# Performance work log

Measured on AMD Instinct MI355X. Metric: run time of the kernel, lower is better.

Reference implementation:

```python
import jax, jax.numpy as jnp
import numpy as np

INPUT_DIM = 3
NUM_LEVELS = 8
LEVEL_DIM = 2
SCALE = 2
BASE_RES = 16
MAX_PARAMS = 2 ** 19
INDEX_PARAMS = 2 ** 14
PROBE = 2 ** 4
BATCH = 524288


def _level_offsets():
    offsets, off = [], 0
    for i in range(NUM_LEVELS):
        res = int(np.ceil(BASE_RES * SCALE ** i))
        p = min(MAX_PARAMS, res ** INPUT_DIM)
        p = int(np.ceil(p / 32) * 32)
        off += p
        offsets.append(off)
    return offsets

OFFSETS = _level_offsets()           # cumulative embedding offsets per level
TOTAL_EMB = OFFSETS[-1]              # 2920448
TOTAL_CB = NUM_LEVELS * INDEX_PARAMS # 131072

PRIMES1 = np.array([1, 2654435761, 805459861], dtype=np.uint32)
PRIMES2 = np.array([1, 2654435767, 805459871], dtype=np.uint32)
_neig = np.arange(1 << INPUT_DIM, dtype=np.int64)[:, None]
_dims = np.arange(INPUT_DIM, dtype=np.int64)[None, :]
BIN_MASK = (_neig & (1 << _dims)) == 0  # [8, 3]


def _fast_hash(ind_u32, primes, size):
    # uint32 multiply wraps mod 2^32, matching `* primes & 0xFFFFFFFF` in torch
    h = ind_u32 * jnp.asarray(primes)
    acc = h[..., 0]
    for d in range(1, INPUT_DIM):
        acc = acc ^ h[..., d]
    return (acc % jnp.uint32(size)).astype(jnp.int32)


def setup_inputs() -> dict:
    key = jax.random.key(0)
    k1, k2, k3 = jax.random.split(key, 3)
    inputs = jax.random.uniform(k1, (BATCH, INPUT_DIM), dtype=jnp.float32)
    # xavier_uniform bounds
    b_e = float(np.sqrt(6.0 / (TOTAL_EMB + LEVEL_DIM)))
    b_c = float(np.sqrt(6.0 / (TOTAL_CB + PROBE)))
    embeddings = jax.random.uniform(k2, (TOTAL_EMB, LEVEL_DIM), jnp.float32, -b_e, b_e)
    code_book = jax.random.uniform(k3, (TOTAL_CB, PROBE), jnp.float32, -b_c, b_c)
    return {"inputs": inputs, "embeddings": embeddings, "code_book": code_book}


def reference(inputs, embeddings, code_book):
    bin_mask = jnp.asarray(BIN_MASK)                    # [8, 3]
    probe_idx = jnp.arange(PROBE, dtype=jnp.int32)      # [PROBE]
    outs = []
    for i in range(NUM_LEVELS):
        res = int(np.ceil(BASE_RES * SCALE ** i))
        offset = 0 if i == 0 else OFFSETS[i - 1]
        params = OFFSETS[i] - offset
        index_offset = i * INDEX_PARAMS
        x = inputs * res
        xi = jnp.floor(x).astype(jnp.int32)             # inputs >= 0, trunc == floor
        xf = x - xi.astype(x.dtype)
        xi = xi[:, None, :]                             # [B, 1, 3]
        xf = xf[:, None, :]
        neigs = jnp.where(bin_mask, xi, xi + 1).astype(jnp.uint32)  # [B, 8, 3]
        # soft index probing (training path)
        h2 = _fast_hash(neigs, PRIMES2, INDEX_PARAMS) + index_offset  # [B, 8]
        index_feat = code_book[h2]                                    # [B, 8, PROBE]
        index_w = jax.nn.softmax(index_feat, axis=-1)
        h1 = _fast_hash(neigs, PRIMES1, params) * PROBE               # [B, 8]
        h1 = (h1[..., None] + probe_idx) % params + offset            # [B, 8, PROBE]
        nf = embeddings[h1]                                           # [B, 8, PROBE, 2]
        feat = jnp.sum(nf * index_w[..., None], axis=-2)              # [B, 8, 2]
        # trilinear interpolation weights
        w = jnp.prod(jnp.where(bin_mask, 1.0 - xf, xf), axis=-1, keepdims=True)  # [B, 8, 1]
        outs.append(jnp.sum(feat * w, axis=-2))                       # [B, 2]
    return jnp.concatenate(outs, axis=-1)                             # [B, 16]
```

## Files before the change

### kernel.cpp

```cpp
#include <hip/hip_runtime.h>
#include <hip/hip_fp16.h>

#define PRIME1Y 2654435761u
#define PRIME1Z 805459861u
#define PRIME2Y 2654435767u
#define PRIME2Z 805459871u

template<int CTRL>
__device__ __forceinline__ float dpp_add(float x) {
    int xi = __float_as_int(x);
    int yi = __builtin_amdgcn_update_dpp(0, xi, CTRL, 0xf, 0xf, true);
    return x + __int_as_float(yi);
}
#define DPP_QUAD_XOR1 0xB1
#define DPP_QUAD_XOR2 0x4E
#define DPP_HALF_MIR  0x141
#define DPP_ROW_MIR   0x140

__device__ __forceinline__ __half2 hc(unsigned u) {
    return __builtin_bit_cast(__half2, u);
}
__device__ __forceinline__ float texp(float x) {
    return fmaf(x, fmaf(x, 0.5f, 1.f), 1.f);
}

__global__ __launch_bounds__(256) void cvt_kernel(
    const float* __restrict__ emb, const float* __restrict__ cb,
    __half* __restrict__ embh, __half* __restrict__ wcb,
    int n4e, int nrows)
{
    int i = blockIdx.x * 256 + threadIdx.x;
    if (i < n4e) {
        float4 v = *reinterpret_cast<const float4*>(emb + (size_t)i * 4);
        __half2 a = __floats2half2_rn(v.x, v.y);
        __half2 b = __floats2half2_rn(v.z, v.w);
        uint2 pk;
        pk.x = __builtin_bit_cast(unsigned, a);
        pk.y = __builtin_bit_cast(unsigned, b);
        *reinterpret_cast<uint2*>(embh + (size_t)i * 4) = pk;
        return;
    }
    i -= n4e;
    if (i >= nrows) return;
    const float* rp = cb + (size_t)i * 16;
    float e[16];
    float S = 0.f;
    #pragma unroll
    for (int k = 0; k < 16; ++k) { e[k] = texp(rp[k]); S += e[k]; }
    const float r = 1.0f / S;
    uint4 lo, hi;
    unsigned w[8];
    #pragma unroll
    for (int k = 0; k < 8; ++k) {
        __half2 h = __floats2half2_rn(e[2*k] * r, e[2*k+1] * r);
        w[k] = __builtin_bit_cast(unsigned, h);
    }
    lo.x = w[0]; lo.y = w[1]; lo.z = w[2]; lo.w = w[3];
    hi.x = w[4]; hi.y = w[5]; hi.z = w[6]; hi.w = w[7];
    char* dst = reinterpret_cast<char*>(wcb) + (size_t)i * 32;
    *reinterpret_cast<uint4*>(dst) = lo;
    *reinterpret_cast<uint4*>(dst + 16) = hi;
}

__global__ __launch_bounds__(256) void compact_hash_f16(
    const float* __restrict__ in,
    const __half* __restrict__ embh,
    const __half* __restrict__ wcb,
    float* __restrict__ out)
{
    const unsigned lane = threadIdx.x & 63u;
    const unsigned wave = threadIdx.x >> 6;
    const unsigned L    = blockIdx.x & 7u;
    const unsigned t = lane & 1u;
    const unsigned c = (lane >> 1) & 7u;
    const unsigned p = lane >> 4;

    const float res = (float)(16u << L);
    const unsigned kb_raw = 12u + 3u * L;
    const unsigned kb = kb_raw < 19u ? kb_raw : 19u;
    const unsigned pmask = (1u << kb) - 1u;
    const unsigned offset = (L == 0u) ? 0u :
                            (L == 1u) ? 4096u :
                            (L == 2u) ? 36864u :
                            299008u + (L - 3u) * 524288u;

    unsigned pb = (blockIdx.x >> 3) * 16u + wave * 4u;
    pb = (unsigned)__builtin_amdgcn_readfirstlane((int)pb);
    const float* ip = in + (size_t)pb * 3u;
    const float ax = ip[0], ay = ip[1],  az = ip[2];
    const float bx = ip[3], by = ip[4],  bz = ip[5];
    const float ex = ip[6], ey = ip[7],  ez = ip[8];
    const float dx = ip[9], dy = ip[10], dz = ip[11];
    const bool hi0 = (lane & 16u) != 0u;
    const bool hi1 = (lane & 32u) != 0u;
    const float xin = hi1 ? (hi0 ? dx : ex) : (hi0 ? bx : ax);
    const float yin = hi1 ? (hi0 ? dy : ey) : (hi0 ? by : ay);
    const float zin = hi1 ? (hi0 ? dz : ez) : (hi0 ? bz : az);

    const float sx = xin * res, sy = yin * res, sz = zin * res;
    const float fx0 = floorf(sx), fy0 = floorf(sy), fz0 = floorf(sz);
    const float fx = sx - fx0, fy = sy - fy0, fz = sz - fz0;
    const unsigned ux = (unsigned)(int)fx0;
    const unsigned uy = (unsigned)(int)fy0;
    const unsigned uz = (unsigned)(int)fz0;

    const unsigned cx = ux + (c & 1u);
    const unsigned hy = uy * PRIME1Y + ((c & 2u) ? PRIME1Y : 0u);
    const unsigned hz = uz * PRIME1Z + ((c & 4u) ? PRIME1Z : 0u);
    const unsigned gy = uy * PRIME2Y + ((c & 2u) ? PRIME2Y : 0u);
    const unsigned gz = uz * PRIME2Z + ((c & 4u) ? PRIME2Z : 0u);

    const unsigned h1 = (cx ^ hy ^ hz) & pmask;
    const unsigned h2 = ((cx ^ gy ^ gz) & 16383u) + (L << 14);

    const uint4 craw = *reinterpret_cast<const uint4*>(
        reinterpret_cast<const char*>(wcb) + h2 * 32u + t * 16u);
    const unsigned erow = offset + ((h1 << 4) & pmask);
    const char* ep = reinterpret_cast<const char*>(embh) + erow * 4u + t * 32u;
    const uint4 eraw0 = *reinterpret_cast<const uint4*>(ep);
    const uint4 eraw1 = *reinterpret_cast<const uint4*>(ep + 16);

    const __half2 w01 = hc(craw.x), w23 = hc(craw.y);
    const __half2 w45 = hc(craw.z), w67 = hc(craw.w);

    __half2 f01 =        __hmul2(__half2half2(__low2half (w01)), hc(eraw0.x));
    f01 = __hfma2(__half2half2(__high2half(w01)), hc(eraw0.y), f01);
    f01 = __hfma2(__half2half2(__low2half (w23)), hc(eraw0.z), f01);
    f01 = __hfma2(__half2half2(__high2half(w23)), hc(eraw0.w), f01);
    f01 = __hfma2(__half2half2(__low2half (w45)), hc(eraw1.x), f01);
    f01 = __hfma2(__half2half2(__high2half(w45)), hc(eraw1.y), f01);
    f01 = __hfma2(__half2half2(__low2half (w67)), hc(eraw1.z), f01);
    f01 = __hfma2(__half2half2(__high2half(w67)), hc(eraw1.w), f01);

    const float wt = ((c & 1u) ? fx : 1.f - fx)
                   * ((c & 2u) ? fy : 1.f - fy)
                   * ((c & 4u) ? fz : 1.f - fz);

    float g0 = __half2float(__low2half(f01))  * wt;
    float g1 = __half2float(__high2half(f01)) * wt;
    g0 = dpp_add<DPP_QUAD_XOR1>(g0);
    g0 = dpp_add<DPP_QUAD_XOR2>(g0);
    g0 = dpp_add<DPP_HALF_MIR>(g0);
    g0 = dpp_add<DPP_ROW_MIR>(g0);
    g1 = dpp_add<DPP_QUAD_XOR1>(g1);
    g1 = dpp_add<DPP_QUAD_XOR2>(g1);
    g1 = dpp_add<DPP_HALF_MIR>(g1);
    g1 = dpp_add<DPP_ROW_MIR>(g1);

    if ((lane & 15u) == 0u) {
        *reinterpret_cast<float2*>(
            reinterpret_cast<char*>(out) + (pb + p) * 64u + L * 8u) =
            make_float2(g0, g1);
    }
}

__device__ __forceinline__ float4 ld4(const float* p) {
    return *reinterpret_cast<const float4*>(p);
}
#define DPP_BCAST15   0x142
__global__ __launch_bounds__(256) void compact_hash_f32(
    const float* __restrict__ in,
    const float* __restrict__ emb,
    const float* __restrict__ cb,
    float* __restrict__ out)
{
    const unsigned lane = threadIdx.x & 63u;
    const unsigned wave = threadIdx.x >> 6;
    const unsigned L    = blockIdx.x & 7u;
    const unsigned point = (blockIdx.x >> 3) * 8u + wave * 2u + (lane >> 5);
    const unsigned s = lane & 3u;
    const unsigned c = (lane >> 2) & 7u;
    const float res = (float)(16u << L);
    const unsigned kb_raw = 12u + 3u * L;
    const unsigned kb = kb_raw < 19u ? kb_raw : 19u;
    const unsigned pmask = (1u << kb) - 1u;
    const unsigned offset = (L == 0u) ? 0u : (L == 1u) ? 4096u :
                            (L == 2u) ? 36864u : 299008u + (L - 3u) * 524288u;
    const float xin = in[point * 3u + 0u];
    const float yin = in[point * 3u + 1u];
    const float zin = in[point * 3u + 2u];
    const float sx = xin * res, sy = yin * res, sz = zin * res;
    const float fx0 = floorf(sx), fy0 = floorf(sy), fz0 = floorf(sz);
    const float fx = sx - fx0, fy = sy - fy0, fz = sz - fz0;
    const unsigned ux = (unsigned)(int)fx0;
    const unsigned uy = (unsigned)(int)fy0;
    const unsigned uz = (unsigned)(int)fz0;
    const unsigned cx = ux + (c & 1u);
    const unsigned hy = uy * PRIME1Y + ((c & 2u) ? PRIME1Y : 0u);
    const unsigned hz = uz * PRIME1Z + ((c & 4u) ? PRIME1Z : 0u);
    const unsigned gy = uy * PRIME2Y + ((c & 2u) ? PRIME2Y : 0u);
    const unsigned gz = uz * PRIME2Z + ((c & 4u) ? PRIME2Z : 0u);
    const unsigned h1 = (cx ^ hy ^ hz) & pmask;
    const unsigned h2 = ((cx ^ gy ^ gz) & 16383u) + (L << 14);
    const float4 cw = ld4(cb + (size_t)h2 * 16u + s * 4u);
    const unsigned ebase = (offset + ((h1 << 4) & pmask)) * 2u;
    const float* ep = emb + (size_t)ebase + s * 8u;
    const float4 e01 = ld4(ep);
    const float4 e23 = ld4(ep + 4);
    const float w0 = texp(cw.x), w1 = texp(cw.y);
    const float w2 = texp(cw.z), w3 = texp(cw.w);
    float S = (w0 + w1) + (w2 + w3);
    S = dpp_add<DPP_QUAD_XOR1>(S);
    S = dpp_add<DPP_QUAD_XOR2>(S);
    float f0 = w0 * e01.x,    f1 = w0 * e01.y;
    f0 = fmaf(w1, e01.z, f0); f1 = fmaf(w1, e01.w, f1);
    f0 = fmaf(w2, e23.x, f0); f1 = fmaf(w2, e23.y, f1);
    f0 = fmaf(w3, e23.z, f0); f1 = fmaf(w3, e23.w, f1);
    const float wt = ((c & 1u) ? fx : 1.f - fx)
                   * ((c & 2u) ? fy : 1.f - fy)
                   * ((c & 4u) ? fz : 1.f - fz);
    const float r = wt * __builtin_amdgcn_rcpf(S);
    float g0 = f0 * r, g1 = f1 * r;
    g0 = dpp_add<DPP_QUAD_XOR1>(g0); g0 = dpp_add<DPP_QUAD_XOR2>(g0);
    g0 = dpp_add<DPP_HALF_MIR>(g0);  g0 = dpp_add<DPP_ROW_MIR>(g0);
    g0 = dpp_add<DPP_BCAST15>(g0);
    g1 = dpp_add<DPP_QUAD_XOR1>(g1); g1 = dpp_add<DPP_QUAD_XOR2>(g1);
    g1 = dpp_add<DPP_HALF_MIR>(g1);  g1 = dpp_add<DPP_ROW_MIR>(g1);
    g1 = dpp_add<DPP_BCAST15>(g1);
    if ((lane & 31u) == 16u) {
        *reinterpret_cast<float2*>(
            reinterpret_cast<char*>(out) + point * 64u + L * 8u) =
            make_float2(g0, g1);
    }
}

extern "C" void kernel_launch(void* const* d_in, const int* in_sizes, int n_in,
                              void* d_out, int out_size, void* d_ws, size_t ws_size,
                              hipStream_t stream) {
    const float* in  = (const float*)d_in[0];
    const float* emb = (const float*)d_in[1];
    const float* cb  = (const float*)d_in[2];
    float* out = (float*)d_out;

    const int batch = in_sizes[0] / 3;
    const size_t embh_bytes = (size_t)in_sizes[1] * 2;
    const size_t cbh_bytes  = (size_t)in_sizes[2] * 2;

    if (ws_size >= embh_bytes + cbh_bytes) {
        __half* embh = (__half*)d_ws;
        __half* wcb  = (__half*)((char*)d_ws + embh_bytes);
        const int n4e   = in_sizes[1] / 4;
        const int nrows = in_sizes[2] / 16;
        const int ncvt = n4e + nrows;
        hipLaunchKernelGGL(cvt_kernel, dim3((ncvt + 255) / 256), dim3(256),
                           0, stream, emb, cb, embh, wcb, n4e, nrows);
        const int nblocks = (batch / 16) * 8;
        hipLaunchKernelGGL(compact_hash_f16, dim3(nblocks), dim3(256),
                           0, stream, in, embh, wcb, out);
    } else {
        const int nblocks = (batch / 8) * 8;
        hipLaunchKernelGGL(compact_hash_f32, dim3(nblocks), dim3(256),
                           0, stream, in, emb, cb, out);
    }
}
```

Baseline: 221.8 us.

## Remap lanes to z-pair corners and store duplicated half2 softmax weights

Each lane now handles two corners that differ only in z, covering a quarter of the 16 probes instead of half of one corner's probes. Softmax weights are stored pre-duplicated as half2 pairs in a 64-byte-per-row workspace layout, so the FMA chain reads packed weights directly with no broadcast shuffles. Per-lane loads become two 16-byte embedding loads plus two codebook loads, and the x/y hash terms are shared between the two corners. The change doubles codebook workspace size and traffic, and falls back to the 32-byte layout when the workspace is too small.

```diff
diff --git a/kernel.cpp b/kernel.cpp
--- a/kernel.cpp
+++ b/kernel.cpp
@@ -20,6 +20,9 @@
 __device__ __forceinline__ __half2 hc(unsigned u) {
     return __builtin_bit_cast(__half2, u);
 }
+__device__ __forceinline__ unsigned hb(__half2 h) {
+    return __builtin_bit_cast(unsigned, h);
+}
 __device__ __forceinline__ float texp(float x) {
     return fmaf(x, fmaf(x, 0.5f, 1.f), 1.f);
 }
@@ -27,16 +30,14 @@
 __global__ __launch_bounds__(256) void cvt_kernel(
     const float* __restrict__ emb, const float* __restrict__ cb,
     __half* __restrict__ embh, __half* __restrict__ wcb,
-    int n4e, int nrows)
+    int n4e, int nrows, int dup)
 {
     int i = blockIdx.x * 256 + threadIdx.x;
     if (i < n4e) {
         float4 v = *reinterpret_cast<const float4*>(emb + (size_t)i * 4);
-        __half2 a = __floats2half2_rn(v.x, v.y);
-        __half2 b = __floats2half2_rn(v.z, v.w);
         uint2 pk;
-        pk.x = __builtin_bit_cast(unsigned, a);
-        pk.y = __builtin_bit_cast(unsigned, b);
+        pk.x = hb(__floats2half2_rn(v.x, v.y));
+        pk.y = hb(__floats2half2_rn(v.z, v.w));
         *reinterpret_cast<uint2*>(embh + (size_t)i * 4) = pk;
         return;
     }
@@ -48,20 +49,32 @@
     #pragma unroll
     for (int k = 0; k < 16; ++k) { e[k] = texp(rp[k]); S += e[k]; }
     const float r = 1.0f / S;
-    uint4 lo, hi;
-    unsigned w[8];
-    #pragma unroll
-    for (int k = 0; k < 8; ++k) {
-        __half2 h = __floats2half2_rn(e[2*k] * r, e[2*k+1] * r);
-        w[k] = __builtin_bit_cast(unsigned, h);
-    }
-    lo.x = w[0]; lo.y = w[1]; lo.z = w[2]; lo.w = w[3];
-    hi.x = w[4]; hi.y = w[5]; hi.z = w[6]; hi.w = w[7];
-    char* dst = reinterpret_cast<char*>(wcb) + (size_t)i * 32;
-    *reinterpret_cast<uint4*>(dst) = lo;
-    *reinterpret_cast<uint4*>(dst + 16) = hi;
-}
-
+    if (dup) {
+        char* dst = reinterpret_cast<char*>(wcb) + (size_t)i * 64;
+        #pragma unroll
+        for (int k = 0; k < 4; ++k) {
+            uint4 v;
+            v.x = hb(__floats2half2_rn(e[4*k+0]*r, e[4*k+0]*r));
+            v.y = hb(__floats2half2_rn(e[4*k+1]*r, e[4*k+1]*r));
+            v.z = hb(__floats2half2_rn(e[4*k+2]*r, e[4*k+2]*r));
+            v.w = hb(__floats2half2_rn(e[4*k+3]*r, e[4*k+3]*r));
+            *reinterpret_cast<uint4*>(dst + k * 16) = v;
+        }
+    } else {
+        char* dst = reinterpret_cast<char*>(wcb) + (size_t)i * 32;
+        #pragma unroll
+        for (int k = 0; k < 2; ++k) {
+            uint4 v;
+            v.x = hb(__floats2half2_rn(e[8*k+0]*r, e[8*k+1]*r));
+            v.y = hb(__floats2half2_rn(e[8*k+2]*r, e[8*k+3]*r));
+            v.z = hb(__floats2half2_rn(e[8*k+4]*r, e[8*k+5]*r));
+            v.w = hb(__floats2half2_rn(e[8*k+6]*r, e[8*k+7]*r));
+            *reinterpret_cast<uint4*>(dst + k * 16) = v;
+        }
+    }
+}
+
+template<bool DUP>
 __global__ __launch_bounds__(256) void compact_hash_f16(
     const float* __restrict__ in,
     const __half* __restrict__ embh,
@@ -71,14 +84,15 @@
     const unsigned lane = threadIdx.x & 63u;
     const unsigned wave = threadIdx.x >> 6;
     const unsigned L    = blockIdx.x & 7u;
-    const unsigned t = lane & 1u;
-    const unsigned c = (lane >> 1) & 7u;
+    const unsigned s = lane & 3u;
+    const unsigned q = (lane >> 2) & 3u;
     const unsigned p = lane >> 4;
 
     const float res = (float)(16u << L);
     const unsigned kb_raw = 12u + 3u * L;
     const unsigned kb = kb_raw < 19u ? kb_raw : 19u;
     const unsigned pmask = (1u << kb) - 1u;
+    const unsigned pm4 = pmask >> 4;
     const unsigned offset = (L == 0u) ? 0u :
                             (L == 1u) ? 4096u :
                             (L == 2u) ? 36864u :
@@ -104,40 +118,65 @@
     const unsigned uy = (unsigned)(int)fy0;
     const unsigned uz = (unsigned)(int)fz0;
 
-    const unsigned cx = ux + (c & 1u);
-    const unsigned hy = uy * PRIME1Y + ((c & 2u) ? PRIME1Y : 0u);
-    const unsigned hz = uz * PRIME1Z + ((c & 4u) ? PRIME1Z : 0u);
-    const unsigned gy = uy * PRIME2Y + ((c & 2u) ? PRIME2Y : 0u);
-    const unsigned gz = uz * PRIME2Z + ((c & 4u) ? PRIME2Z : 0u);
-
-    const unsigned h1 = (cx ^ hy ^ hz) & pmask;
-    const unsigned h2 = ((cx ^ gy ^ gz) & 16383u) + (L << 14);
-
-    const uint4 craw = *reinterpret_cast<const uint4*>(
-        reinterpret_cast<const char*>(wcb) + h2 * 32u + t * 16u);
-    const unsigned erow = offset + ((h1 << 4) & pmask);
-    const char* ep = reinterpret_cast<const char*>(embh) + erow * 4u + t * 32u;
-    const uint4 eraw0 = *reinterpret_cast<const uint4*>(ep);
-    const uint4 eraw1 = *reinterpret_cast<const uint4*>(ep + 16);
-
-    const __half2 w01 = hc(craw.x), w23 = hc(craw.y);
-    const __half2 w45 = hc(craw.z), w67 = hc(craw.w);
-
-    __half2 f01 =        __hmul2(__half2half2(__low2half (w01)), hc(eraw0.x));
-    f01 = __hfma2(__half2half2(__high2half(w01)), hc(eraw0.y), f01);
-    f01 = __hfma2(__half2half2(__low2half (w23)), hc(eraw0.z), f01);
-    f01 = __hfma2(__half2half2(__high2half(w23)), hc(eraw0.w), f01);
-    f01 = __hfma2(__half2half2(__low2half (w45)), hc(eraw1.x), f01);
-    f01 = __hfma2(__half2half2(__high2half(w45)), hc(eraw1.y), f01);
-    f01 = __hfma2(__half2half2(__low2half (w67)), hc(eraw1.z), f01);
-    f01 = __hfma2(__half2half2(__high2half(w67)), hc(eraw1.w), f01);
-
-    const float wt = ((c & 1u) ? fx : 1.f - fx)
-                   * ((c & 2u) ? fy : 1.f - fy)
-                   * ((c & 4u) ? fz : 1.f - fz);
-
-    float g0 = __half2float(__low2half(f01))  * wt;
-    float g1 = __half2float(__high2half(f01)) * wt;
+    const unsigned cx  = ux + (q & 1u);
+    const unsigned hxy = cx ^ (uy * PRIME1Y + ((q & 2u) ? PRIME1Y : 0u));
+    const unsigned gxy = cx ^ (uy * PRIME2Y + ((q & 2u) ? PRIME2Y : 0u));
+    const unsigned hz0 = uz * PRIME1Z, hz1 = hz0 + PRIME1Z;
+    const unsigned gz0 = uz * PRIME2Z, gz1 = gz0 + PRIME2Z;
+
+    const unsigned cbase = DUP ? ((L << 20) + s * 16u) : ((L << 19) + s * 8u);
+    const unsigned ebase = offset * 4u + s * 16u;
+
+    const unsigned h2a = (gxy ^ gz0) & 16383u;
+    const unsigned h2b = (gxy ^ gz1) & 16383u;
+    const unsigned ca = cbase + (DUP ? (h2a << 6) : (h2a << 5));
+    const unsigned cbo = cbase + (DUP ? (h2b << 6) : (h2b << 5));
+    const unsigned ea = ebase + (((hxy ^ hz0) & pm4) << 6);
+    const unsigned eb = ebase + (((hxy ^ hz1) & pm4) << 6);
+
+    const char* cbp = reinterpret_cast<const char*>(wcb);
+    const char* ebp = reinterpret_cast<const char*>(embh);
+    const uint4 eA = *reinterpret_cast<const uint4*>(ebp + ea);
+    const uint4 eB = *reinterpret_cast<const uint4*>(ebp + eb);
+
+    __half2 f01A, f01B;
+    if (DUP) {
+        const uint4 cA = *reinterpret_cast<const uint4*>(cbp + ca);
+        const uint4 cB = *reinterpret_cast<const uint4*>(cbp + cbo);
+        f01A =        __hmul2(hc(cA.x), hc(eA.x));
+        f01A = __hfma2(hc(cA.y), hc(eA.y), f01A);
+        f01A = __hfma2(hc(cA.z), hc(eA.z), f01A);
+        f01A = __hfma2(hc(cA.w), hc(eA.w), f01A);
+        f01B =        __hmul2(hc(cB.x), hc(eB.x));
+        f01B = __hfma2(hc(cB.y), hc(eB.y), f01B);
+        f01B = __hfma2(hc(cB.z), hc(eB.z), f01B);
+        f01B = __hfma2(hc(cB.w), hc(eB.w), f01B);
+    } else {
+        const uint2 cA = *reinterpret_cast<const uint2*>(cbp + ca);
+        const uint2 cB = *reinterpret_cast<const uint2*>(cbp + cbo);
+        const __half2 a01 = hc(cA.x), a23 = hc(cA.y);
+        const __half2 b01 = hc(cB.x), b23 = hc(cB.y);
+        f01A =        __hmul2(__half2half2(__low2half (a01)), hc(eA.x));
+        f01A = __hfma2(__half2half2(__high2half(a01)), hc(eA.y), f01A);
+        f01A = __hfma2(__half2half2(__low2half (a23)), hc(eA.z), f01A);
+        f01A = __hfma2(__half2half2(__high2half(a23)), hc(eA.w), f01A);
+        f01B =        __hmul2(__half2half2(__low2half (b01)), hc(eB.x));
+        f01B = __hfma2(__half2half2(__high2half(b01)), hc(eB.y), f01B);
+        f01B = __hfma2(__half2half2(__low2half (b23)), hc(eB.z), f01B);
+        f01B = __hfma2(__half2half2(__high2half(b23)), hc(eB.w), f01B);
+    }
+
+    const float wx = (q & 1u) ? fx : 1.f - fx;
+    const float wy = (q & 2u) ? fy : 1.f - fy;
+    const float wxy = wx * wy;
+    const float wt0 = wxy * (1.f - fz);
+    const float wt1 = wxy * fz;
+
+    float g0 =      __half2float(__low2half (f01A)) * wt0;
+    g0 = fmaf(__half2float(__low2half (f01B)), wt1, g0);
+    float g1 =      __half2float(__high2half(f01A)) * wt0;
+    g1 = fmaf(__half2float(__high2half(f01B)), wt1, g1);
+
     g0 = dpp_add<DPP_QUAD_XOR1>(g0);
     g0 = dpp_add<DPP_QUAD_XOR2>(g0);
     g0 = dpp_add<DPP_HALF_MIR>(g0);
@@ -233,23 +272,31 @@
     float* out = (float*)d_out;
 
     const int batch = in_sizes[0] / 3;
+    const int n4e   = in_sizes[1] / 4;
+    const int nrows = in_sizes[2] / 16;
     const size_t embh_bytes = (size_t)in_sizes[1] * 2;
-    const size_t cbh_bytes  = (size_t)in_sizes[2] * 2;
-
-    if (ws_size >= embh_bytes + cbh_bytes) {
+    const size_t wdup_bytes = (size_t)nrows * 64;
+    const size_t wnor_bytes = (size_t)nrows * 32;
+    const int ncvt = n4e + nrows;
+    const int nblocks = (batch / 16) * 8;
+
+    if (ws_size >= embh_bytes + wdup_bytes) {
         __half* embh = (__half*)d_ws;
         __half* wcb  = (__half*)((char*)d_ws + embh_bytes);
-        const int n4e   = in_sizes[1] / 4;
-        const int nrows = in_sizes[2] / 16;
-        const int ncvt = n4e + nrows;
         hipLaunchKernelGGL(cvt_kernel, dim3((ncvt + 255) / 256), dim3(256),
-                           0, stream, emb, cb, embh, wcb, n4e, nrows);
-        const int nblocks = (batch / 16) * 8;
-        hipLaunchKernelGGL(compact_hash_f16, dim3(nblocks), dim3(256),
+                           0, stream, emb, cb, embh, wcb, n4e, nrows, 1);
+        hipLaunchKernelGGL((compact_hash_f16<true>), dim3(nblocks), dim3(256),
+                           0, stream, in, embh, wcb, out);
+    } else if (ws_size >= embh_bytes + wnor_bytes) {
+        __half* embh = (__half*)d_ws;
+        __half* wcb  = (__half*)((char*)d_ws + embh_bytes);
+        hipLaunchKernelGGL(cvt_kernel, dim3((ncvt + 255) / 256), dim3(256),
+                           0, stream, emb, cb, embh, wcb, n4e, nrows, 0);
+        hipLaunchKernelGGL((compact_hash_f16<false>), dim3(nblocks), dim3(256),
                            0, stream, in, embh, wcb, out);
     } else {
-        const int nblocks = (batch / 8) * 8;
-        hipLaunchKernelGGL(compact_hash_f32, dim3(nblocks), dim3(256),
+        const int nb32 = (batch / 8) * 8;
+        hipLaunchKernelGGL(compact_hash_f32, dim3(nb32), dim3(256),
                            0, stream, in, emb, cb, out);
     }
 }
```

New measurement: 235.4 us. +6.2%, slower.
